# Optimization experiments

Hardware: AMD Instinct MI355X
Metric: run time of the kernel (lower is better)

The kernel has to match this reference:

```python
import jax, jax.numpy as jnp
import numpy as np

# Concrete segmented polynomial: one operation, channelwise tensor product.
# N nodes, E edges, U channels, S spherical-harmonic dim; output per node = U*S.
N, U, S = 100000, 32, 4
E = 3_200_000  # N * avg_degree(32)


def setup_inputs() -> dict:
    key = jax.random.key(0)
    k1, k2, k3, k4 = jax.random.split(key, 4)
    return {
        "x": jax.random.normal(k1, (N, U), dtype=jnp.float32),    # node features (input buffer 0)
        "sh": jax.random.normal(k2, (E, S), dtype=jnp.float32),   # per-edge spherical harmonics (input buffer 1)
        "src": jax.random.randint(k3, (E,), 0, N),                 # input_indices[0]
        "dst": jax.random.randint(k4, (E,), 0, N),                 # output_indices[0]
    }


def reference(x, sh, src, dst):
    # 1) indexed gather: inputs[0] = inputs[0][input_indices[0]]
    xg = x[src]                                         # [E, U]
    # 2) fx-generated einsum tensor product (operand moved last): 'eu,es->eus'
    msg = (xg[:, :, None] * sh[:, None, :]).reshape(E, U * S)  # [E, U*S]
    # 3) scatter_add into zero-initialized output buffer [N, U*S]
    out = jax.ops.segment_sum(msg, dst, num_segments=N)  # [N, U*S]
    return out
```

## Files before the change

kernel.cpp:

```cpp
#include <hip/hip_runtime.h>


#define U_DIM 32
#define US 128

__device__ inline unsigned f2bf(float f) {
    unsigned u = __float_as_uint(f);
    return (u + 0x7FFF + ((u >> 16) & 1)) >> 16;
}
__device__ inline float bfl(unsigned w) { return __uint_as_float(w << 16); }
__device__ inline float bfh(unsigned w) { return __uint_as_float(w & 0xFFFF0000u); }

__global__ void __launch_bounds__(256) xcvt_kernel(
        const float4* __restrict__ x4, ushort4* __restrict__ xb4, int n4) {
    int i = blockIdx.x * 256 + threadIdx.x;
    if (i < n4) {
        float4 v = x4[i];
        ushort4 r;
        r.x = (unsigned short)f2bf(v.x);
        r.y = (unsigned short)f2bf(v.y);
        r.z = (unsigned short)f2bf(v.z);
        r.w = (unsigned short)f2bf(v.w);
        xb4[i] = r;
    }
}

#define C1_LOG 9
#define C1_NPB 512
#define C1_MAXK 256
#define C1_NBLK 256
#define FINE_LOG 7
#define FINE_NPB 128
#define KF_MAX 1024
#define SCAP 5120

__global__ void __launch_bounds__(1024) c1_hist_kernel(
        const int* __restrict__ dst, int* __restrict__ ccount_f,
        int* __restrict__ cnt, int E, int KF, int K1, int EPB) {
    __shared__ int h[KF_MAX];
    for (int b = threadIdx.x; b < KF; b += 1024) h[b] = 0;
    __syncthreads();
    int base = blockIdx.x * EPB;
    int lim = min(EPB, E - base);
    for (int i = threadIdx.x; i < lim; i += 1024)
        atomicAdd(&h[dst[base + i] >> FINE_LOG], 1);
    __syncthreads();
    for (int b = threadIdx.x; b < KF; b += 1024) {
        int c = h[b];
        if (c) atomicAdd(&ccount_f[b], c);
    }
    for (int b = threadIdx.x; b < K1; b += 1024) {
        int c = 0;
        #pragma unroll
        for (int k = 0; k < 4; ++k) {
            int f = 4 * b + k;
            if (f < KF) c += h[f];
        }
        cnt[b * C1_NBLK + blockIdx.x] = c;
    }
}

__global__ void __launch_bounds__(1024) c1_scan_kernel(
        const int* __restrict__ ccount_f, int* __restrict__ fbase,
        int* __restrict__ cbase, int* __restrict__ offsets,
        int KF, int K1, int N, int E) {
    __shared__ int sc[1024];
    int t = threadIdx.x;
    int v = (t < KF) ? ccount_f[t] : 0;
    sc[t] = v;
    __syncthreads();
    for (int off = 1; off < 1024; off <<= 1) {
        int w = (t >= off) ? sc[t - off] : 0;
        __syncthreads();
        sc[t] += w;
        __syncthreads();
    }
    if (t < KF) fbase[t] = sc[t] - v;
    __syncthreads();
    if (t < K1) {
        int f = 4 * t;
        cbase[t] = (f < KF) ? (sc[f] - ccount_f[f]) : E;
    }
    if (t == 0) { fbase[KF] = E; cbase[K1] = E; offsets[N] = E; }
}

__global__ void __launch_bounds__(C1_NBLK) c1_cbase_kernel(
        const int* __restrict__ cnt, const int* __restrict__ cbase,
        int* __restrict__ base_tab) {
    __shared__ int sc[C1_NBLK];
    int b = blockIdx.x;
    int t = threadIdx.x;
    int v = cnt[b * C1_NBLK + t];
    sc[t] = v;
    __syncthreads();
    for (int off = 1; off < C1_NBLK; off <<= 1) {
        int w = (t >= off) ? sc[t - off] : 0;
        __syncthreads();
        sc[t] += w;
        __syncthreads();
    }
    base_tab[b * C1_NBLK + t] = cbase[b] + sc[t] - v;
}

__global__ void __launch_bounds__(1024) c1_scatter_kernel(
        const int* __restrict__ dst, const int* __restrict__ src,
        const float4* __restrict__ sh, const int* __restrict__ base_tab,
        uint2* __restrict__ pay8A, int* __restrict__ packedA,
        int E, int K1, int EPB) {
    __shared__ int cur[C1_MAXK];
    for (int b = threadIdx.x; b < K1; b += 1024)
        cur[b] = base_tab[b * C1_NBLK + blockIdx.x];
    __syncthreads();
    int base = blockIdx.x * EPB;
    int lim = min(EPB, E - base);
    for (int i = threadIdx.x; i < lim; i += 1024) {
        int e = base + i;
        int d = dst[e];
        int b = d >> C1_LOG;
        int pos = atomicAdd(&cur[b], 1);
        float4 s4 = sh[e];
        pay8A[pos] = make_uint2(f2bf(s4.x) | (f2bf(s4.y) << 16),
                                f2bf(s4.z) | (f2bf(s4.w) << 16));
        packedA[pos] = ((d & (C1_NPB - 1)) << 21) | src[e];
    }
}

__global__ void __launch_bounds__(512) c2_sort_kernel(
        const int* __restrict__ cbase, const int* __restrict__ fbase,
        int* __restrict__ offsets, const uint2* __restrict__ pay8A,
        const int* __restrict__ packedA, uint2* __restrict__ pay8B,
        int* __restrict__ packedB, int N) {
    __shared__ uint2 spay[SCAP];
    __shared__ int   spk[SCAP];
    __shared__ int   hh[FINE_NPB];
    __shared__ int   scur[FINE_NPB];
    int fb = blockIdx.x;
    int t = threadIdx.x;
    int parent = fb >> 2, sub = fb & 3;
    int cbeg = cbase[parent], cend = cbase[parent + 1];
    int fbeg = fbase[fb];
    int cnt = fbase[fb + 1] - fbeg;
    if (t < FINE_NPB) hh[t] = 0;
    __syncthreads();
    for (int i = cbeg + t; i < cend; i += 512) {
        int nc = (packedA[i] >> 21) & (C1_NPB - 1);
        if ((nc >> FINE_LOG) == sub)
            atomicAdd(&hh[nc & (FINE_NPB - 1)], 1);
    }
    __syncthreads();
    int v = (t < FINE_NPB) ? hh[t] : 0;
    if (t < FINE_NPB) hh[t] = v;
    __syncthreads();
    for (int off = 1; off < FINE_NPB; off <<= 1) {
        int w = (t < FINE_NPB && t >= off) ? hh[t - off] : 0;
        __syncthreads();
        if (t < FINE_NPB) hh[t] += w;
        __syncthreads();
    }
    if (t < FINE_NPB) {
        int excl = hh[t] - v;
        scur[t] = excl;
        int node = (fb << FINE_LOG) + t;
        if (node < N) offsets[node] = fbeg + excl;
    }
    __syncthreads();
    for (int i = cbeg + t; i < cend; i += 512) {
        int pk = packedA[i];
        int nc = (pk >> 21) & (C1_NPB - 1);
        if ((nc >> FINE_LOG) == sub) {
            int pos = atomicAdd(&scur[nc & (FINE_NPB - 1)], 1);
            uint2 p8 = pay8A[i];
            if (pos < SCAP) { spk[pos] = pk; spay[pos] = p8; }
            else { packedB[fbeg + pos] = pk; pay8B[fbeg + pos] = p8; }
        }
    }
    __syncthreads();
    int lim = min(cnt, SCAP);
    for (int i = t; i < lim; i += 512) {
        packedB[fbeg + i] = spk[i];
        pay8B[fbeg + i] = spay[i];
    }
}

__global__ void __launch_bounds__(256) accum_kernel(
        const unsigned short* __restrict__ xb, const uint2* __restrict__ pay8,
        const int* __restrict__ packed, const int* __restrict__ offsets,
        float* __restrict__ out, int smask, int N) {
    int wave = threadIdx.x >> 6;
    int lane = threadIdx.x & 63;
    int grp = lane >> 4;
    int l = lane & 15;
    int n = blockIdx.x * 16 + wave * 4 + grp;
    if (n >= N) return;
    int beg = offsets[n], end = offsets[n + 1];
    int u2 = l << 1;
    float a0 = 0.f, a1 = 0.f, a2 = 0.f, a3 = 0.f;
    float a4 = 0.f, a5 = 0.f, a6 = 0.f, a7 = 0.f;
    int i = beg;
    for (; i + 3 < end; i += 4) {
        int pk0 = packed[i], pk1 = packed[i + 1];
        int pk2 = packed[i + 2], pk3 = packed[i + 3];
        uint2 q0 = pay8[i], q1 = pay8[i + 1];
        uint2 q2 = pay8[i + 2], q3 = pay8[i + 3];
        ushort2 xv0 = *reinterpret_cast<const ushort2*>(
            &xb[(size_t)(pk0 & smask) * U_DIM + u2]);
        ushort2 xv1 = *reinterpret_cast<const ushort2*>(
            &xb[(size_t)(pk1 & smask) * U_DIM + u2]);
        ushort2 xv2 = *reinterpret_cast<const ushort2*>(
            &xb[(size_t)(pk2 & smask) * U_DIM + u2]);
        ushort2 xv3 = *reinterpret_cast<const ushort2*>(
            &xb[(size_t)(pk3 & smask) * U_DIM + u2]);
        {
            float xa = bfl((unsigned)xv0.x), xc = bfl((unsigned)xv0.y);
            float s0 = bfl(q0.x), s1 = bfh(q0.x), s2 = bfl(q0.y), s3 = bfh(q0.y);
            a0 += xa * s0; a1 += xa * s1; a2 += xa * s2; a3 += xa * s3;
            a4 += xc * s0; a5 += xc * s1; a6 += xc * s2; a7 += xc * s3;
        }
        {
            float xa = bfl((unsigned)xv1.x), xc = bfl((unsigned)xv1.y);
            float s0 = bfl(q1.x), s1 = bfh(q1.x), s2 = bfl(q1.y), s3 = bfh(q1.y);
            a0 += xa * s0; a1 += xa * s1; a2 += xa * s2; a3 += xa * s3;
            a4 += xc * s0; a5 += xc * s1; a6 += xc * s2; a7 += xc * s3;
        }
        {
            float xa = bfl((unsigned)xv2.x), xc = bfl((unsigned)xv2.y);
            float s0 = bfl(q2.x), s1 = bfh(q2.x), s2 = bfl(q2.y), s3 = bfh(q2.y);
            a0 += xa * s0; a1 += xa * s1; a2 += xa * s2; a3 += xa * s3;
            a4 += xc * s0; a5 += xc * s1; a6 += xc * s2; a7 += xc * s3;
        }
        {
            float xa = bfl((unsigned)xv3.x), xc = bfl((unsigned)xv3.y);
            float s0 = bfl(q3.x), s1 = bfh(q3.x), s2 = bfl(q3.y), s3 = bfh(q3.y);
            a0 += xa * s0; a1 += xa * s1; a2 += xa * s2; a3 += xa * s3;
            a4 += xc * s0; a5 += xc * s1; a6 += xc * s2; a7 += xc * s3;
        }
    }
    for (; i < end; ++i) {
        int pk = packed[i];
        uint2 q = pay8[i];
        ushort2 xv = *reinterpret_cast<const ushort2*>(
            &xb[(size_t)(pk & smask) * U_DIM + u2]);
        float xa = bfl((unsigned)xv.x), xc = bfl((unsigned)xv.y);
        float s0 = bfl(q.x), s1 = bfh(q.x), s2 = bfl(q.y), s3 = bfh(q.y);
        a0 += xa * s0; a1 += xa * s1; a2 += xa * s2; a3 += xa * s3;
        a4 += xc * s0; a5 += xc * s1; a6 += xc * s2; a7 += xc * s3;
    }
    size_t obase = (size_t)n * US + (size_t)u2 * 4;
    *reinterpret_cast<float4*>(&out[obase])     = make_float4(a0, a1, a2, a3);
    *reinterpret_cast<float4*>(&out[obase + 4]) = make_float4(a4, a5, a6, a7);
}

#define LOG_NPBK 7
#define NPBK 128
#define MAXK 1024
#define NBLK 256
#define CAP 5120
#define SPILL_E 1000000

__global__ void __launch_bounds__(1024) coarse_hist_kernel(
        const int* __restrict__ dst, int* __restrict__ ccount,
        int* __restrict__ cnt, int E, int K, int EPB) {
    __shared__ int h[MAXK];
    for (int b = threadIdx.x; b < K; b += 1024) h[b] = 0;
    __syncthreads();
    int base = blockIdx.x * EPB;
    int lim = min(EPB, E - base);
    for (int i = threadIdx.x; i < lim; i += 1024)
        atomicAdd(&h[dst[base + i] >> LOG_NPBK], 1);
    __syncthreads();
    for (int b = threadIdx.x; b < K; b += 1024) {
        int c = h[b];
        cnt[b * NBLK + blockIdx.x] = c;
        if (c) atomicAdd(&ccount[b], c);
    }
}

__global__ void __launch_bounds__(1024) coarse_scan_kernel(
        const int* __restrict__ ccount, int* __restrict__ cbase,
        int* __restrict__ offsets, int* __restrict__ spill_cursor,
        int K, int N, int E) {
    __shared__ int sc[1024];
    int t = threadIdx.x;
    int v = (t < K) ? ccount[t] : 0;
    sc[t] = v;
    __syncthreads();
    for (int off = 1; off < 1024; off <<= 1) {
        int w = (t >= off) ? sc[t - off] : 0;
        __syncthreads();
        sc[t] += w;
        __syncthreads();
    }
    if (t < K) cbase[t] = sc[t] - v;
    if (t == 0) { cbase[K] = E; offsets[N] = E; *spill_cursor = 0; }
}

__global__ void __launch_bounds__(NBLK) chunk_base_kernel(
        const int* __restrict__ cnt, const int* __restrict__ cbase,
        int* __restrict__ base_tab) {
    __shared__ int sc[NBLK];
    int b = blockIdx.x;
    int t = threadIdx.x;
    int v = cnt[b * NBLK + t];
    sc[t] = v;
    __syncthreads();
    for (int off = 1; off < NBLK; off <<= 1) {
        int w = (t >= off) ? sc[t - off] : 0;
        __syncthreads();
        sc[t] += w;
        __syncthreads();
    }
    base_tab[b * NBLK + t] = cbase[b] + sc[t] - v;
}

__global__ void __launch_bounds__(1024) coarse_scatter_kernel(
        const int* __restrict__ dst, const int* __restrict__ src,
        const float4* __restrict__ sh, const int* __restrict__ base_tab,
        uint2* __restrict__ pay8, int* __restrict__ packed,
        int E, int K, int EPB) {
    __shared__ int cur[MAXK];
    for (int b = threadIdx.x; b < K; b += 1024)
        cur[b] = base_tab[b * NBLK + blockIdx.x];
    __syncthreads();
    int base = blockIdx.x * EPB;
    int lim = min(EPB, E - base);
    for (int i = threadIdx.x; i < lim; i += 1024) {
        int e = base + i;
        int d = dst[e];
        int b = d >> LOG_NPBK;
        int pos = atomicAdd(&cur[b], 1);
        float4 s4 = sh[e];
        pay8[pos] = make_uint2(f2bf(s4.x) | (f2bf(s4.y) << 16),
                               f2bf(s4.z) | (f2bf(s4.w) << 16));
        packed[pos] = ((d & (NPBK - 1)) << 24) | src[e];
    }
}

__global__ void __launch_bounds__(512) fine_sort_kernel(
        const int* __restrict__ cbase, int* __restrict__ offsets,
        uint2* __restrict__ pay8, int* __restrict__ packed,
        uint2* __restrict__ spill_pay, int* __restrict__ spill_pk,
        int* __restrict__ spill_cursor, int N) {
    __shared__ uint2 spay[CAP];
    __shared__ int   spk[CAP];
    __shared__ int   cnt_[NPBK];
    __shared__ int   sc[NPBK];
    __shared__ int   sbase_s;
    int b = blockIdx.x;
    int t = threadIdx.x;
    int cbeg = cbase[b], cend = cbase[b + 1];
    int cnt = cend - cbeg;
    if (t == 0) sbase_s = (cnt > CAP) ? atomicAdd(spill_cursor, cnt - CAP) : 0;
    if (t < NPBK) cnt_[t] = 0;
    __syncthreads();
    for (int i = t; i < cnt; i += 512) {
        int pk = packed[cbeg + i];
        uint2 p8 = pay8[cbeg + i];
        atomicAdd(&cnt_[(pk >> 24) & (NPBK - 1)], 1);
        if (i < CAP) { spk[i] = pk; spay[i] = p8; }
        else {
            int sp = sbase_s + (i - CAP);
            if (sp < SPILL_E) { spill_pk[sp] = pk; spill_pay[sp] = p8; }
        }
    }
    __syncthreads();
    int v = (t < NPBK) ? cnt_[t] : 0;
    if (t < NPBK) sc[t] = v;
    __syncthreads();
    for (int off = 1; off < NPBK; off <<= 1) {
        int w = (t < NPBK && t >= off) ? sc[t - off] : 0;
        __syncthreads();
        if (t < NPBK) sc[t] += w;
        __syncthreads();
    }
    if (t < NPBK) {
        int ex = sc[t] - v;
        int node = (b << LOG_NPBK) + t;
        if (node <= N) offsets[node] = cbeg + ex;
        cnt_[t] = ex;
    }
    __syncthreads();
    for (int i = t; i < cnt; i += 512) {
        int pk; uint2 p8;
        bool ok = true;
        if (i < CAP) { pk = spk[i]; p8 = spay[i]; }
        else {
            int sp = sbase_s + (i - CAP);
            ok = (sp < SPILL_E);
            if (ok) { pk = spill_pk[sp]; p8 = spill_pay[sp]; }
        }
        if (ok) {
            int pos = cbeg + atomicAdd(&cnt_[(pk >> 24) & (NPBK - 1)], 1);
            packed[pos] = pk;
            pay8[pos] = p8;
        }
    }
}

constexpr int SCAN_BLOCK = 256;
constexpr int SCAN_ITEMS = 8;
constexpr int SCAN_CHUNK = SCAN_BLOCK * SCAN_ITEMS;

__global__ void __launch_bounds__(256) hist_kernel(
        const int* __restrict__ dst, int* __restrict__ counts, int E) {
    int e = blockIdx.x * blockDim.x + threadIdx.x;
    if (e < E) atomicAdd(&counts[dst[e]], 1);
}
__global__ void __launch_bounds__(SCAN_BLOCK) block_sum_kernel(
        const int* __restrict__ counts, int* __restrict__ bsums, int N) {
    __shared__ int sdata[SCAN_BLOCK];
    int base = blockIdx.x * SCAN_CHUNK;
    int sum = 0;
    for (int j = 0; j < SCAN_ITEMS; ++j) {
        int idx = base + j * SCAN_BLOCK + threadIdx.x;
        if (idx < N) sum += counts[idx];
    }
    sdata[threadIdx.x] = sum;
    __syncthreads();
    for (int off = SCAN_BLOCK / 2; off > 0; off >>= 1) {
        if (threadIdx.x < off) sdata[threadIdx.x] += sdata[threadIdx.x + off];
        __syncthreads();
    }
    if (threadIdx.x == 0) bsums[blockIdx.x] = sdata[0];
}
__global__ void scan_bsums_kernel(int* __restrict__ bsums, int nb) {
    if (threadIdx.x == 0 && blockIdx.x == 0) {
        int acc = 0;
        for (int i = 0; i < nb; ++i) { int v = bsums[i]; bsums[i] = acc; acc += v; }
    }
}
__global__ void __launch_bounds__(SCAN_BLOCK) scan_final_kernel(
        const int* __restrict__ counts, const int* __restrict__ bsums,
        int* __restrict__ offsets, int* __restrict__ cursors, int N, int E) {
    __shared__ int sdata[SCAN_BLOCK];
    int base = blockIdx.x * SCAN_CHUNK + threadIdx.x * SCAN_ITEMS;
    int local[SCAN_ITEMS];
    int tsum = 0;
    for (int j = 0; j < SCAN_ITEMS; ++j) {
        int idx = base + j;
        int v = (idx < N) ? counts[idx] : 0;
        local[j] = tsum;
        tsum += v;
    }
    sdata[threadIdx.x] = tsum;
    __syncthreads();
    for (int off = 1; off < SCAN_BLOCK; off <<= 1) {
        int v = (threadIdx.x >= off) ? sdata[threadIdx.x - off] : 0;
        __syncthreads();
        sdata[threadIdx.x] += v;
        __syncthreads();
    }
    int excl = sdata[threadIdx.x] - tsum + bsums[blockIdx.x];
    for (int j = 0; j < SCAN_ITEMS; ++j) {
        int idx = base + j;
        if (idx < N) { int o = excl + local[j]; offsets[idx] = o; cursors[idx] = o; }
    }
    if (blockIdx.x == 0 && threadIdx.x == 0) offsets[N] = E;
}
__global__ void __launch_bounds__(256) scatter_ids_kernel(
        const int* __restrict__ dst, int* __restrict__ cursors,
        int* __restrict__ eids, int E) {
    int e = blockIdx.x * blockDim.x + threadIdx.x;
    if (e < E) { int pos = atomicAdd(&cursors[dst[e]], 1); eids[pos] = e; }
}
__global__ void __launch_bounds__(US) accum_ids_kernel(
        const float* __restrict__ x, const float* __restrict__ sh,
        const int* __restrict__ src, const int* __restrict__ offsets,
        const int* __restrict__ eids, float* __restrict__ out) {
    int n = blockIdx.x;
    int t = threadIdx.x;
    int u = t >> 2, s = t & 3;
    int beg = offsets[n], end = offsets[n + 1];
    float acc = 0.f;
    for (int i = beg; i < end; ++i) {
        int e = eids[i];
        acc += x[src[e] * U_DIM + u] * sh[e * 4 + s];
    }
    out[(size_t)n * US + t] = acc;
}
__global__ void __launch_bounds__(US) atomic_kernel(
        const float* __restrict__ x, const float* __restrict__ sh,
        const int* __restrict__ src, const int* __restrict__ dst,
        float* __restrict__ out, int E) {
    int e = blockIdx.x;
    int t = threadIdx.x;
    float v = x[src[e] * U_DIM + (t >> 2)] * sh[e * 4 + (t & 3)];
    atomicAdd(&out[(size_t)dst[e] * US + t], v);
}

extern "C" void kernel_launch(void* const* d_in, const int* in_sizes, int n_in,
                              void* d_out, int out_size, void* d_ws, size_t ws_size,
                              hipStream_t stream) {
    const float* x  = (const float*)d_in[0];
    const float* sh = (const float*)d_in[1];
    const int* src  = (const int*)d_in[2];
    const int* dst  = (const int*)d_in[3];
    float* out = (float*)d_out;

    const int E = in_sizes[2];
    const int N = in_sizes[0] / U_DIM;
    const int xn4 = in_sizes[0] / 4;
    const int egrid = (E + 255) / 256;
    const int nb = (N + SCAN_CHUNK - 1) / SCAN_CHUNK;

    const int K1 = (N + C1_NPB - 1) >> C1_LOG;
    const int KF = (N + FINE_NPB - 1) >> FINE_LOG;
    const int EPB1 = (E + C1_NBLK - 1) / C1_NBLK;
    size_t need_main = (size_t)E * 24 + (size_t)in_sizes[0] * 2 +
                       (size_t)(N + 1 + 2 * KF + 2 + K1 + 1 +
                                2 * K1 * C1_NBLK) * 4;

    const int K = (N + NPBK - 1) >> LOG_NPBK;
    const int EPB = (E + NBLK - 1) / NBLK;
    size_t need_r7 = (size_t)E * 12 + (size_t)SPILL_E * 12 + (size_t)(N + 1) * 4 +
                     (size_t)(2 * K + 2) * 4 + (size_t)(2 * K * NBLK) * 4 +
                     (size_t)in_sizes[0] * 2;
    size_t need_ids = (size_t)E * 4 + (size_t)(3 * N + 1 + nb) * 4;

    if (K1 <= C1_MAXK && KF <= KF_MAX && N <= (1 << 21) &&
        (in_sizes[0] % 4 == 0) && ws_size >= need_main) {
        uint2* pay8A   = (uint2*)d_ws;
        uint2* pay8B   = pay8A + E;
        int* packedA   = (int*)(pay8B + E);
        int* packedB   = packedA + E;
        unsigned short* xb = (unsigned short*)(packedB + E);
        int* offsets   = (int*)(xb + in_sizes[0]);
        int* ccount_f  = offsets + N + 1;
        int* fbase     = ccount_f + KF;
        int* cbase     = fbase + KF + 1;
        int* cnt       = cbase + K1 + 1;
        int* base_tab  = cnt + K1 * C1_NBLK;

        hipMemsetAsync(ccount_f, 0, sizeof(int) * (size_t)KF, stream);
        xcvt_kernel<<<(xn4 + 255) / 256, 256, 0, stream>>>(
            (const float4*)x, (ushort4*)xb, xn4);
        c1_hist_kernel<<<C1_NBLK, 1024, 0, stream>>>(dst, ccount_f, cnt,
                                                     E, KF, K1, EPB1);
        c1_scan_kernel<<<1, 1024, 0, stream>>>(ccount_f, fbase, cbase, offsets,
                                               KF, K1, N, E);
        c1_cbase_kernel<<<K1, C1_NBLK, 0, stream>>>(cnt, cbase, base_tab);
        c1_scatter_kernel<<<C1_NBLK, 1024, 0, stream>>>(dst, src, (const float4*)sh,
                                                        base_tab, pay8A, packedA,
                                                        E, K1, EPB1);
        c2_sort_kernel<<<KF, 512, 0, stream>>>(cbase, fbase, offsets,
                                               pay8A, packedA, pay8B, packedB, N);
        accum_kernel<<<(N + 15) / 16, 256, 0, stream>>>(xb, pay8B, packedB,
                                                        offsets, out, 0x1FFFFF, N);
    } else if (K <= MAXK && (in_sizes[0] % 4 == 0) && ws_size >= need_r7) {
        uint2* pay8      = (uint2*)d_ws;
        uint2* spill_pay = pay8 + E;
        int* packed      = (int*)(spill_pay + SPILL_E);
        int* spill_pk    = packed + E;
        int* offsets     = spill_pk + SPILL_E;
        int* ccount      = offsets + N + 1;
        int* cbase       = ccount + K;
        int* cnt         = cbase + K + 1;
        int* base_tab    = cnt + K * NBLK;
        int* spill_cur   = base_tab + K * NBLK;
        unsigned short* xb = (unsigned short*)(spill_cur + 1);

        hipMemsetAsync(ccount, 0, sizeof(int) * (size_t)K, stream);
        xcvt_kernel<<<(xn4 + 255) / 256, 256, 0, stream>>>(
            (const float4*)x, (ushort4*)xb, xn4);
        coarse_hist_kernel<<<NBLK, 1024, 0, stream>>>(dst, ccount, cnt, E, K, EPB);
        coarse_scan_kernel<<<1, 1024, 0, stream>>>(ccount, cbase, offsets,
                                                   spill_cur, K, N, E);
        chunk_base_kernel<<<K, NBLK, 0, stream>>>(cnt, cbase, base_tab);
        coarse_scatter_kernel<<<NBLK, 1024, 0, stream>>>(dst, src, (const float4*)sh,
                                                         base_tab, pay8, packed,
                                                         E, K, EPB);
        fine_sort_kernel<<<K, 512, 0, stream>>>(cbase, offsets, pay8, packed,
                                                spill_pay, spill_pk, spill_cur, N);
        accum_kernel<<<(N + 15) / 16, 256, 0, stream>>>(xb, pay8, packed,
                                                        offsets, out, 0xFFFFFF, N);
    } else if (ws_size >= need_ids) {
        int* eids    = (int*)d_ws;
        int* counts  = eids + E;
        int* offsets = counts + N;
        int* cursors = offsets + N + 1;
        int* bsums   = cursors + N;

        hipMemsetAsync(counts, 0, sizeof(int) * (size_t)N, stream);
        hist_kernel<<<egrid, 256, 0, stream>>>(dst, counts, E);
        block_sum_kernel<<<nb, SCAN_BLOCK, 0, stream>>>(counts, bsums, N);
        scan_bsums_kernel<<<1, 64, 0, stream>>>(bsums, nb);
        scan_final_kernel<<<nb, SCAN_BLOCK, 0, stream>>>(counts, bsums, offsets, cursors, N, E);
        scatter_ids_kernel<<<egrid, 256, 0, stream>>>(dst, cursors, eids, E);
        accum_ids_kernel<<<N, US, 0, stream>>>(x, sh, src, offsets, eids, out);
    } else {
        hipMemsetAsync(out, 0, sizeof(float) * (size_t)out_size, stream);
        atomic_kernel<<<E, US, 0, stream>>>(x, sh, src, dst, out, E);
    }
}
```

Measured before the change: 201.7 us.

## Stage coarse scatter through LDS local sort for coalesced global writes

The coarse bucket scatter kernel now handles edges in chunks of 4096. Each chunk is counting-sorted by bucket in shared memory with a local histogram, a prefix scan and shared atomics, and then written out in sorted order. Consecutive threads therefore write contiguous runs in each bucket's global region, replacing fully random scattered stores. The cost is extra shared memory (about 53KB), several barriers per chunk and a serial scan, which may reduce occupancy.

Measured after the change: 194.5 us. 1.04x faster.

```diff
diff --git a/kernel.cpp b/kernel.cpp
--- a/kernel.cpp
+++ b/kernel.cpp
@@ -33,6 +33,7 @@
 #define FINE_NPB 128
 #define KF_MAX 1024
 #define SCAP 5120
+#define SCH 4096
 
 __global__ void __launch_bounds__(1024) c1_hist_kernel(
         const int* __restrict__ dst, int* __restrict__ ccount_f,
@@ -107,21 +108,77 @@
         const float4* __restrict__ sh, const int* __restrict__ base_tab,
         uint2* __restrict__ pay8A, int* __restrict__ packedA,
         int E, int K1, int EPB) {
-    __shared__ int cur[C1_MAXK];
-    for (int b = threadIdx.x; b < K1; b += 1024)
-        cur[b] = base_tab[b * C1_NBLK + blockIdx.x];
-    __syncthreads();
+    __shared__ uint2 spay[SCH];
+    __shared__ int   spk[SCH];
+    __shared__ unsigned char sbkt[SCH];
+    __shared__ int   hist[C1_MAXK];
+    __shared__ int   lo[C1_MAXK];
+    __shared__ int   scur[C1_MAXK];
+    __shared__ int   gcur[C1_MAXK];
+    __shared__ int   sc[C1_MAXK];
+    int t = threadIdx.x;
+    for (int b = t; b < K1; b += 1024)
+        gcur[b] = base_tab[b * C1_NBLK + blockIdx.x];
     int base = blockIdx.x * EPB;
     int lim = min(EPB, E - base);
-    for (int i = threadIdx.x; i < lim; i += 1024) {
-        int e = base + i;
-        int d = dst[e];
-        int b = d >> C1_LOG;
-        int pos = atomicAdd(&cur[b], 1);
-        float4 s4 = sh[e];
-        pay8A[pos] = make_uint2(f2bf(s4.x) | (f2bf(s4.y) << 16),
-                                f2bf(s4.z) | (f2bf(s4.w) << 16));
-        packedA[pos] = ((d & (C1_NPB - 1)) << 21) | src[e];
+
+    for (int sb = 0; sb < lim; sb += SCH) {
+        int sublen = min(SCH, lim - sb);
+        for (int b = t; b < K1; b += 1024) hist[b] = 0;
+        __syncthreads();
+        int bk[4], pk[4];
+        uint2 pv[4];
+        bool vld[4];
+        #pragma unroll
+        for (int k = 0; k < 4; ++k) {
+            int idx = t + k * 1024;
+            vld[k] = (idx < sublen);
+            if (vld[k]) {
+                int e = base + sb + idx;
+                int d = dst[e];
+                bk[k] = d >> C1_LOG;
+                float4 s4 = sh[e];
+                pv[k] = make_uint2(f2bf(s4.x) | (f2bf(s4.y) << 16),
+                                   f2bf(s4.z) | (f2bf(s4.w) << 16));
+                pk[k] = ((d & (C1_NPB - 1)) << 21) | src[e];
+                atomicAdd(&hist[bk[k]], 1);
+            }
+        }
+        __syncthreads();
+        if (t < C1_MAXK) sc[t] = (t < K1) ? hist[t] : 0;
+        __syncthreads();
+        for (int off = 1; off < C1_MAXK; off <<= 1) {
+            int w = 0;
+            if (t < C1_MAXK && t >= off) w = sc[t - off];
+            __syncthreads();
+            if (t < C1_MAXK) sc[t] += w;
+            __syncthreads();
+        }
+        if (t < C1_MAXK) {
+            int excl = sc[t] - ((t < K1) ? hist[t] : 0);
+            lo[t] = excl;
+            scur[t] = excl;
+        }
+        __syncthreads();
+        #pragma unroll
+        for (int k = 0; k < 4; ++k) {
+            if (vld[k]) {
+                int pos = atomicAdd(&scur[bk[k]], 1);
+                spk[pos] = pk[k];
+                spay[pos] = pv[k];
+                sbkt[pos] = (unsigned char)bk[k];
+            }
+        }
+        __syncthreads();
+        for (int i = t; i < sublen; i += 1024) {
+            int b = sbkt[i];
+            int gd = gcur[b] + (i - lo[b]);
+            packedA[gd] = spk[i];
+            pay8A[gd] = spay[i];
+        }
+        __syncthreads();
+        if (t < K1) gcur[t] += hist[t];
+        __syncthreads();
     }
 }
 
```
